# Kernel tuning notes

Measured on AMD Instinct MI355X. Metric: run time of the kernel, lower is better.

Reference implementation:

```python
import jax, jax.numpy as jnp
import numpy as np
from jax import lax

D_MODEL, N_STATE, L_LEN = 1024, 64, 4096
DT_INIT = 0.1


def hippo_legs_matrix(N):
    # Standard HiPPO-LegS: A[n,k] = -sqrt(2n+1)sqrt(2k+1) if n>k, -(n+1) if n==k, 0 else
    n = np.arange(N, dtype=np.float32)
    r = np.sqrt(2.0 * n + 1.0)
    A = np.where(n[:, None] > n[None, :], r[:, None] * r[None, :], 0.0)
    A = -(A + np.diag(n + 1.0))
    B = r.copy()
    return jnp.asarray(A, jnp.float32), jnp.asarray(B, jnp.float32)


def setup_inputs() -> dict:
    key = jax.random.key(0)
    kB, kC = jax.random.split(key)
    A_ct, B_ref = hippo_legs_matrix(N_STATE)
    B0 = jnp.tile(B_ref[None, :], (D_MODEL, 1))
    B = B0 + 0.01 * jax.random.normal(kB, (D_MODEL, N_STATE), jnp.float32)
    C = jax.random.normal(kC, (D_MODEL, N_STATE), jnp.float32) * 0.1
    D = jnp.zeros((D_MODEL,), jnp.float32)
    log_dt = jnp.asarray(np.log(DT_INIT), jnp.float32)
    return {"A_ct": A_ct, "B": B, "C": C, "D": D, "log_dt": log_dt}


def reference(A_ct, B, C, D, log_dt):
    dt = jnp.exp(log_dt)
    N = A_ct.shape[0]
    I = jnp.eye(N, dtype=A_ct.dtype)
    M = I - (dt / 2.0) * A_ct          # (N,N)
    P = I + (dt / 2.0) * A_ct          # (N,N)
    A_bar = jnp.linalg.solve(M, P)     # (N,N)
    # B_bar[d] = M^{-1} (dt * B[d])  -> solve on transposed batch
    B_bar = jnp.linalg.solve(M, (dt * B).T).T  # (D,N)

    def step(x, _):
        # x: (D,N) state; emit readout then advance
        y = jnp.sum(C * x, axis=-1)    # (D,)
        return x @ A_bar.T, y

    _, ys = lax.scan(step, B_bar, None, length=L_LEN)  # ys: (L,D)
    K = ys.T                                           # (D,L)
    K = K.at[:, 0].add(D)
    return K[:, None, :]                                # (D,1,L)
```

## Files before the change

### kernel.cpp

```cpp
#include <hip/hip_runtime.h>
#include <math.h>


#define BPAD 72

#define WS_BBAR   16
#define WS_SPL    65552
#define WS_MV     (WS_SPL + 12*8192)
#define WS_GT     (WS_MV + 4096)
#define WS_H      (WS_GT + 64*4096)
#define WS_W      (WS_H + 64*4096)
#define WS_X      (WS_W + 1024*4096)

using bf16x8 = __attribute__((ext_vector_type(8))) short;
using f32x4v = __attribute__((ext_vector_type(4))) float;
typedef unsigned short ushort_t;

__device__ __forceinline__ ushort_t f2bf(float x) {
  unsigned u = __builtin_bit_cast(unsigned, x);
  return (ushort_t)((u + 0x7FFFu + ((u >> 16) & 1u)) >> 16);
}
__device__ __forceinline__ float bfhi(float x) {
  unsigned u = __builtin_bit_cast(unsigned, x);
  unsigned r = (u + 0x7FFFu + ((u >> 16) & 1u)) & 0xFFFF0000u;
  return __builtin_bit_cast(float, r);
}
__device__ __forceinline__ ushort_t* usp(float* ws, int foff) {
  return (ushort_t*)(ws + foff);
}
__device__ __forceinline__ const ushort_t* uspc(const float* ws, int foff) {
  return (const ushort_t*)(ws + foff);
}

__device__ __forceinline__ void mm_frag(const ushort_t* __restrict__ Ah,
                                        const ushort_t* __restrict__ Al,
                                        const ushort_t* __restrict__ Bh,
                                        const ushort_t* __restrict__ Bl,
                                        int w, int lane, f32x4v acc[4]) {
  const int lm = lane & 15, quad = lane >> 4;
  const int ar = (16 * w + lm) * BPAD, ko = quad * 8;
#pragma unroll
  for (int nt = 0; nt < 4; ++nt) { acc[nt][0] = acc[nt][1] = acc[nt][2] = acc[nt][3] = 0.f; }
#pragma unroll
  for (int kc = 0; kc < 64; kc += 32) {
    const bf16x8 ahi = *(const bf16x8*)&Ah[ar + kc + ko];
    const bf16x8 alo = *(const bf16x8*)&Al[ar + kc + ko];
#pragma unroll
    for (int nt = 0; nt < 4; ++nt) {
      const int br = (16 * nt + lm) * BPAD + kc + ko;
      const bf16x8 bhi = *(const bf16x8*)&Bh[br];
      const bf16x8 blo = *(const bf16x8*)&Bl[br];
      acc[nt] = __builtin_amdgcn_mfma_f32_16x16x32_bf16(ahi, bhi, acc[nt], 0, 0, 0);
      acc[nt] = __builtin_amdgcn_mfma_f32_16x16x32_bf16(ahi, blo, acc[nt], 0, 0, 0);
      acc[nt] = __builtin_amdgcn_mfma_f32_16x16x32_bf16(alo, bhi, acc[nt], 0, 0, 0);
    }
  }
}

__device__ __forceinline__ void dstore_lds(const f32x4v acc[4],
                                           ushort_t* __restrict__ Ah, ushort_t* __restrict__ Al,
                                           ushort_t* __restrict__ Bth, ushort_t* __restrict__ Btl,
                                           int w, int lane) {
  const int lm = lane & 15, quad = lane >> 4;
#pragma unroll
  for (int nt = 0; nt < 4; ++nt) {
    const int n = 16 * nt + lm;
#pragma unroll
    for (int reg = 0; reg < 4; ++reg) {
      const int m = 16 * w + 4 * quad + reg;
      const float x = acc[nt][reg];
      const ushort_t h = f2bf(x), l = f2bf(x - bfhi(x));
      Ah[m * BPAD + n] = h; Al[m * BPAD + n] = l;
      Bth[n * BPAD + m] = h; Btl[n * BPAD + m] = l;
    }
  }
}

__device__ __forceinline__ void cp_l2w(const ushort_t* __restrict__ l,
                                       ushort_t* __restrict__ g, int tid) {
  for (int e = tid; e < 512; e += 256) {
    const int row = e >> 3, c8 = (e & 7) * 8;
    *(uint4*)&g[row * 64 + c8] = *(const uint4*)&l[row * BPAD + c8];
  }
}
__device__ __forceinline__ void cp_w2l(const ushort_t* __restrict__ g,
                                       ushort_t* __restrict__ l, int tid) {
  for (int e = tid; e < 512; e += 256) {
    const int row = e >> 3, c8 = (e & 7) * 8;
    *(uint4*)&l[row * BPAD + c8] = *(const uint4*)&g[row * 64 + c8];
  }
}

__device__ __forceinline__ void split_stage(const float* __restrict__ g,
                                            ushort_t* __restrict__ Ah,
                                            ushort_t* __restrict__ Al, int tid) {
#pragma unroll
  for (int j = 0; j < 4; ++j) {
    const int flat = j * 1024 + tid * 4;
    const int row = flat >> 6, col = flat & 63;
    const float4 v = *(const float4*)&g[flat];
    ushort_t h0 = f2bf(v.x), h1 = f2bf(v.y), h2 = f2bf(v.z), h3 = f2bf(v.w);
    ushort_t l0 = f2bf(v.x - bfhi(v.x)), l1 = f2bf(v.y - bfhi(v.y));
    ushort_t l2 = f2bf(v.z - bfhi(v.z)), l3 = f2bf(v.w - bfhi(v.w));
    uint2 hp, lp;
    hp.x = (unsigned)h0 | ((unsigned)h1 << 16); hp.y = (unsigned)h2 | ((unsigned)h3 << 16);
    lp.x = (unsigned)l0 | ((unsigned)l1 << 16); lp.y = (unsigned)l2 | ((unsigned)l3 << 16);
    *(uint2*)&Ah[row * BPAD + col] = hp;
    *(uint2*)&Al[row * BPAD + col] = lp;
  }
}

#define ARR (64 * BPAD)

__global__ __launch_bounds__(256) void k_setup(const float* __restrict__ A,
                                               const float* __restrict__ logdt,
                                               float* __restrict__ ws) {
  __shared__ __align__(16) char SM[74240];
  float* Msh = (float*)SM;
  float* Tm  = (float*)(SM + 16640);
  float* tmpb = (float*)(SM + 33280);
  ushort_t* ping = (ushort_t*)(SM + 37376);
  ushort_t* pong = (ushort_t*)SM;
  const int tid = threadIdx.x;
  const int w = tid >> 6, lane = tid & 63;

  const float hdt = 0.5f * expf(logdt[0]);
  for (int idx = tid; idx < 4096; idx += 256) {
    const int i = idx >> 6, j = idx & 63;
    Msh[i * 65 + j] = ((i == j) ? 1.f : 0.f) - hdt * A[idx];
    Tm[i * 65 + j] = 0.f;
  }
  __syncthreads();
  if (tid < 64) Tm[tid * 65 + tid] = 1.0f / Msh[tid * 65 + tid];
  __syncthreads();
  for (int lb = 0; lb < 6; ++lb) {
    const int b = 1 << lb;
    const int E = 32 * b;
    for (int e = tid; e < E; e += 256) {
      const int rem = e & (b * b - 1);
      const int p = e >> (2 * lb);
      const int i = rem >> lb, j = rem & (b - 1);
      const int c0 = p << (lb + 1), r0 = c0 + b;
      float s = 0.f;
      for (int k = 0; k < b; ++k)
        s += Msh[(r0 + i) * 65 + c0 + k] * Tm[(c0 + k) * 65 + c0 + j];
      tmpb[e] = s;
    }
    __syncthreads();
    for (int e = tid; e < E; e += 256) {
      const int rem = e & (b * b - 1);
      const int p = e >> (2 * lb);
      const int i = rem >> lb, j = rem & (b - 1);
      const int c0 = p << (lb + 1), r0 = c0 + b;
      float s = 0.f;
      const float* tp = &tmpb[e - rem];
      for (int k = 0; k < b; ++k)
        s += Tm[(r0 + i) * 65 + r0 + k] * tp[k * b + j];
      Tm[(r0 + i) * 65 + c0 + j] = -s;
    }
    __syncthreads();
  }

  {
    ushort_t* MvH = usp(ws, WS_MV);
    ushort_t* MvL = usp(ws, WS_MV + 2048);
    for (int idx = tid; idx < 4096; idx += 256) {
      const int i = idx >> 6, j = idx & 63;
      const float mv = Tm[i * 65 + j];
      MvH[idx] = f2bf(mv); MvL[idx] = f2bf(mv - bfhi(mv));
      const float v = 2.f * mv - ((i == j) ? 1.f : 0.f);
      const ushort_t h = f2bf(v), l = f2bf(v - bfhi(v));
      ping[0 * ARR + i * BPAD + j] = h; ping[1 * ARR + i * BPAD + j] = l;
      ping[2 * ARR + j * BPAD + i] = h; ping[3 * ARR + j * BPAD + i] = l;
    }
  }
  __syncthreads();
  cp_l2w(ping + 0 * ARR, usp(ws, WS_SPL + 0), tid);
  cp_l2w(ping + 1 * ARR, usp(ws, WS_SPL + 2048), tid);
  cp_l2w(ping + 2 * ARR, usp(ws, WS_SPL + 4096), tid);
  cp_l2w(ping + 3 * ARR, usp(ws, WS_SPL + 6144), tid);

  ushort_t* cur = ping;
  ushort_t* nxt = pong;
  for (int sj = 1; sj < 12; ++sj) {
    f32x4v acc[4];
    mm_frag(cur, cur + ARR, cur + 2 * ARR, cur + 3 * ARR, w, lane, acc);
    dstore_lds(acc, nxt, nxt + ARR, nxt + 2 * ARR, nxt + 3 * ARR, w, lane);
    __syncthreads();
    const int base = WS_SPL + sj * 8192;
    cp_l2w(nxt + 0 * ARR, usp(ws, base + 0), tid);
    cp_l2w(nxt + 1 * ARR, usp(ws, base + 2048), tid);
    cp_l2w(nxt + 2 * ARR, usp(ws, base + 4096), tid);
    cp_l2w(nxt + 3 * ARR, usp(ws, base + 6144), tid);
    ushort_t* t = cur; cur = nxt; nxt = t;
  }
}

__global__ __launch_bounds__(256) void k_powers(const float* __restrict__ Bg,
                                                const float* __restrict__ logdt,
                                                float* __restrict__ ws) {
  __shared__ __align__(16) ushort_t SMp[8 * ARR];
  ushort_t* curA = SMp;
  ushort_t* ponA = SMp + 2 * ARR;
  ushort_t* Bst  = SMp + 4 * ARR;
  ushort_t* BtO  = SMp + 6 * ARR;
  const int p = blockIdx.x, tid = threadIdx.x;
  const int w = tid >> 6, lane = tid & 63;

  if (p < 128) {
    const int chain = p >> 6, r = p & 63;
    ushort_t* dstH = usp(ws, (chain ? WS_H : WS_GT) + r * 4096);
    ushort_t* dstL = usp(ws, (chain ? WS_H : WS_GT) + r * 4096 + 2048);
    if (r == 0) {
      for (int idx = tid; idx < 4096; idx += 256) {
        const int i = idx >> 6, j = idx & 63;
        dstH[idx] = (i == j) ? (ushort_t)0x3F80 : (ushort_t)0;
        dstL[idx] = 0;
      }
      return;
    }
    const int j0 = __ffs(r) - 1;
    if (r == (1 << j0)) {
      const int sb = WS_SPL + (chain * 6 + j0) * 8192;
      const int src = chain ? sb : (sb + 4096);
      const uint4* sh = (const uint4*)uspc(ws, src);
      const uint4* sl = (const uint4*)uspc(ws, src + 2048);
      uint4* dh = (uint4*)dstH;
      uint4* dl = (uint4*)dstL;
      for (int e = tid; e < 512; e += 256) { dh[e] = sh[e]; dl[e] = sl[e]; }
      return;
    }
    {
      const int sb = WS_SPL + (chain * 6 + j0) * 8192;
      cp_w2l(uspc(ws, sb + 0), curA, tid);
      cp_w2l(uspc(ws, sb + 2048), curA + ARR, tid);
    }
    ushort_t* ca = curA;
    ushort_t* na = ponA;
    for (int j = j0 + 1; j < 6; ++j) {
      if ((r >> j) & 1) {
        __syncthreads();
        const int sb = WS_SPL + (chain * 6 + j) * 8192;
        cp_w2l(uspc(ws, sb + 4096), Bst, tid);
        cp_w2l(uspc(ws, sb + 6144), Bst + ARR, tid);
        __syncthreads();
        f32x4v acc[4];
        mm_frag(ca, ca + ARR, Bst, Bst + ARR, w, lane, acc);
        dstore_lds(acc, na, na + ARR, BtO, BtO + ARR, w, lane);
        ushort_t* t = ca; ca = na; na = t;
      }
    }
    __syncthreads();
    if (chain == 0) {
      cp_l2w(BtO, dstH, tid);
      cp_l2w(BtO + ARR, dstL, tid);
    } else {
      cp_l2w(ca, dstH, tid);
      cp_l2w(ca + ARR, dstL, tid);
    }
  } else {
    const int d0 = (p - 128) * 64;
    const float dtv = expf(logdt[0]);
    split_stage(Bg + d0 * 64, curA, curA + ARR, tid);
    cp_w2l(uspc(ws, WS_MV), Bst, tid);
    cp_w2l(uspc(ws, WS_MV + 2048), Bst + ARR, tid);
    __syncthreads();
    f32x4v acc[4];
    mm_frag(curA, curA + ARR, Bst, Bst + ARR, w, lane, acc);
    const int lm = lane & 15, quad = lane >> 4;
    float* od = ws + WS_BBAR + d0 * 64;
#pragma unroll
    for (int nt = 0; nt < 4; ++nt)
#pragma unroll
      for (int reg = 0; reg < 4; ++reg)
        od[(16 * w + 4 * quad + reg) * 64 + 16 * nt + lm] = dtv * acc[nt][reg];
  }
}

__global__ __launch_bounds__(256) void k_expand(const float* __restrict__ Cg,
                                                float* __restrict__ ws) {
  __shared__ __align__(16) ushort_t SMe[4 * ARR];
  ushort_t* Asp = SMe;
  ushort_t* Bsp = SMe + 2 * ARR;
  const int p = blockIdx.x, tid = threadIdx.x;
  const int chain = p >> 10, rr = (p >> 4) & 63, dch = p & 15;
  const int w = tid >> 6, lane = tid & 63;
  const int d0 = dch * 64;

  split_stage(chain ? (ws + WS_BBAR + d0 * 64) : (Cg + d0 * 64), Asp, Asp + ARR, tid);
  const int mb = (chain ? WS_H : WS_GT) + rr * 4096;
  cp_w2l(uspc(ws, mb + 0), Bsp, tid);
  cp_w2l(uspc(ws, mb + 2048), Bsp + ARR, tid);
  __syncthreads();

  f32x4v acc[4];
  mm_frag(Asp, Asp + ARR, Bsp, Bsp + ARR, w, lane, acc);

  const int lm = lane & 15, quad = lane >> 4;
  float* dst = ws + (chain ? WS_X : WS_W) + d0 * 4096 + rr * 64;
#pragma unroll
  for (int nt = 0; nt < 4; ++nt)
#pragma unroll
    for (int reg = 0; reg < 4; ++reg)
      dst[(16 * w + 4 * quad + reg) * 4096 + 16 * nt + lm] = acc[nt][reg];
}

__global__ __launch_bounds__(256) void k_contract(const float* __restrict__ Dg,
                                                  const float* __restrict__ ws,
                                                  float* __restrict__ out) {
  __shared__ __align__(16) ushort_t XhiL[64 * BPAD];
  __shared__ __align__(16) ushort_t XloL[64 * BPAD];
  __shared__ __align__(16) ushort_t WhiL[64 * BPAD];
  __shared__ __align__(16) ushort_t WloL[64 * BPAD];
  const int d = blockIdx.x, tid = threadIdx.x;
  const float* Wg = ws + WS_W + d * 4096;
  const float* Xg = ws + WS_X + d * 4096;

#pragma unroll
  for (int j = 0; j < 4; ++j) {
    const int flat = j * 1024 + tid * 4;
    const int row = flat >> 6, col = flat & 63;
    const float4 wv = *(const float4*)&Wg[flat];
    const float4 xv = *(const float4*)&Xg[flat];
    const int o = row * BPAD + col;
#pragma unroll
    for (int s = 0; s < 2; ++s) {
      const float4 v = s ? xv : wv;
      ushort_t h0 = f2bf(v.x), h1 = f2bf(v.y), h2 = f2bf(v.z), h3 = f2bf(v.w);
      ushort_t l0 = f2bf(v.x - bfhi(v.x)), l1 = f2bf(v.y - bfhi(v.y));
      ushort_t l2 = f2bf(v.z - bfhi(v.z)), l3 = f2bf(v.w - bfhi(v.w));
      uint2 hp, lp;
      hp.x = (unsigned)h0 | ((unsigned)h1 << 16); hp.y = (unsigned)h2 | ((unsigned)h3 << 16);
      lp.x = (unsigned)l0 | ((unsigned)l1 << 16); lp.y = (unsigned)l2 | ((unsigned)l3 << 16);
      *(uint2*)&(s ? XhiL : WhiL)[o] = hp;
      *(uint2*)&(s ? XloL : WloL)[o] = lp;
    }
  }
  __syncthreads();

  const int w = tid >> 6, lane = tid & 63;
  const int lm = lane & 15, quad = lane >> 4;
  const int qrow = 16 * w + lm;
  const int koff = quad * 8;

  f32x4v acc[4];
#pragma unroll
  for (int nt = 0; nt < 4; ++nt) { acc[nt][0] = 0.f; acc[nt][1] = 0.f; acc[nt][2] = 0.f; acc[nt][3] = 0.f; }

#pragma unroll
  for (int kc = 0; kc < 64; kc += 32) {
    const bf16x8 ahi = *(const bf16x8*)&XhiL[qrow * BPAD + kc + koff];
    const bf16x8 alo = *(const bf16x8*)&XloL[qrow * BPAD + kc + koff];
#pragma unroll
    for (int nt = 0; nt < 4; ++nt) {
      const int rrow = 16 * nt + lm;
      const bf16x8 bhi = *(const bf16x8*)&WhiL[rrow * BPAD + kc + koff];
      const bf16x8 blo = *(const bf16x8*)&WloL[rrow * BPAD + kc + koff];
      acc[nt] = __builtin_amdgcn_mfma_f32_16x16x32_bf16(ahi, bhi, acc[nt], 0, 0, 0);
      acc[nt] = __builtin_amdgcn_mfma_f32_16x16x32_bf16(ahi, blo, acc[nt], 0, 0, 0);
      acc[nt] = __builtin_amdgcn_mfma_f32_16x16x32_bf16(alo, bhi, acc[nt], 0, 0, 0);
    }
  }

  if (tid == 0) acc[0][0] += Dg[d];

  float* od = out + d * 4096;
#pragma unroll
  for (int nt = 0; nt < 4; ++nt) {
#pragma unroll
    for (int reg = 0; reg < 4; ++reg) {
      const int q = 16 * w + quad * 4 + reg;
      od[q * 64 + 16 * nt + lm] = acc[nt][reg];
    }
  }
}

extern "C" void kernel_launch(void* const* d_in, const int* in_sizes, int n_in,
                              void* d_out, int out_size, void* d_ws, size_t ws_size,
                              hipStream_t stream) {
  const float* A     = (const float*)d_in[0];
  const float* B     = (const float*)d_in[1];
  const float* C     = (const float*)d_in[2];
  const float* Dv    = (const float*)d_in[3];
  const float* logdt = (const float*)d_in[4];
  float* ws  = (float*)d_ws;
  float* out = (float*)d_out;

  hipLaunchKernelGGL(k_setup,    dim3(1),    dim3(256), 0, stream, A, logdt, ws);
  hipLaunchKernelGGL(k_powers,   dim3(144),  dim3(256), 0, stream, B, logdt, ws);
  hipLaunchKernelGGL(k_expand,   dim3(2048), dim3(256), 0, stream, C, ws);
  hipLaunchKernelGGL(k_contract, dim3(1024), dim3(256), 0, stream, Dv, ws, out);
}
```

Measured before the change: 127.9 us.

## Load MFMA fragments directly from global memory and reuse B tiles in expand

Removes LDS staging across k_powers, k_expand and k_contract: MFMA operand fragments are now loaded straight from global or workspace memory and split into bf16 hi/lo in registers via a new helper. k_expand now keeps the power-matrix fragments in registers and loops over four d-chunks per block, so its grid shrinks from 2048 to 512 blocks. dstore_lds packs its transposed stores into uint2 writes. The change drops LDS round-trips and barriers, but in exchange it relies on uncoalesced global loads and gives expand less parallelism.

```diff
diff --git a/kernel.cpp b/kernel.cpp
--- a/kernel.cpp
+++ b/kernel.cpp
@@ -3,6 +3,7 @@
 
 
 #define BPAD 72
+#define ARR (64 * BPAD)
 
 #define WS_BBAR   16
 #define WS_SPL    65552
@@ -32,6 +33,18 @@
   return (const ushort_t*)(ws + foff);
 }
 
+__device__ __forceinline__ void ldsplit8(const float* __restrict__ p,
+                                         bf16x8& h, bf16x8& l) {
+  const float4 a = *(const float4*)p;
+  const float4 b = *(const float4*)(p + 4);
+  const float v[8] = {a.x, a.y, a.z, a.w, b.x, b.y, b.z, b.w};
+#pragma unroll
+  for (int i = 0; i < 8; ++i) {
+    h[i] = (short)f2bf(v[i]);
+    l[i] = (short)f2bf(v[i] - bfhi(v[i]));
+  }
+}
+
 __device__ __forceinline__ void mm_frag(const ushort_t* __restrict__ Ah,
                                         const ushort_t* __restrict__ Al,
                                         const ushort_t* __restrict__ Bh,
@@ -62,17 +75,25 @@
                                            ushort_t* __restrict__ Bth, ushort_t* __restrict__ Btl,
                                            int w, int lane) {
   const int lm = lane & 15, quad = lane >> 4;
+  const int m0 = 16 * w + 4 * quad;
 #pragma unroll
   for (int nt = 0; nt < 4; ++nt) {
     const int n = 16 * nt + lm;
+    ushort_t h[4], l[4];
 #pragma unroll
     for (int reg = 0; reg < 4; ++reg) {
-      const int m = 16 * w + 4 * quad + reg;
       const float x = acc[nt][reg];
-      const ushort_t h = f2bf(x), l = f2bf(x - bfhi(x));
-      Ah[m * BPAD + n] = h; Al[m * BPAD + n] = l;
-      Bth[n * BPAD + m] = h; Btl[n * BPAD + m] = l;
-    }
+      h[reg] = f2bf(x); l[reg] = f2bf(x - bfhi(x));
+      Ah[(m0 + reg) * BPAD + n] = h[reg];
+      Al[(m0 + reg) * BPAD + n] = l[reg];
+    }
+    uint2 hp, lp;
+    hp.x = (unsigned)h[0] | ((unsigned)h[1] << 16);
+    hp.y = (unsigned)h[2] | ((unsigned)h[3] << 16);
+    lp.x = (unsigned)l[0] | ((unsigned)l[1] << 16);
+    lp.y = (unsigned)l[2] | ((unsigned)l[3] << 16);
+    *(uint2*)&Bth[n * BPAD + m0] = hp;
+    *(uint2*)&Btl[n * BPAD + m0] = lp;
   }
 }
 
@@ -83,34 +104,6 @@
     *(uint4*)&g[row * 64 + c8] = *(const uint4*)&l[row * BPAD + c8];
   }
 }
-__device__ __forceinline__ void cp_w2l(const ushort_t* __restrict__ g,
-                                       ushort_t* __restrict__ l, int tid) {
-  for (int e = tid; e < 512; e += 256) {
-    const int row = e >> 3, c8 = (e & 7) * 8;
-    *(uint4*)&l[row * BPAD + c8] = *(const uint4*)&g[row * 64 + c8];
-  }
-}
-
-__device__ __forceinline__ void split_stage(const float* __restrict__ g,
-                                            ushort_t* __restrict__ Ah,
-                                            ushort_t* __restrict__ Al, int tid) {
-#pragma unroll
-  for (int j = 0; j < 4; ++j) {
-    const int flat = j * 1024 + tid * 4;
-    const int row = flat >> 6, col = flat & 63;
-    const float4 v = *(const float4*)&g[flat];
-    ushort_t h0 = f2bf(v.x), h1 = f2bf(v.y), h2 = f2bf(v.z), h3 = f2bf(v.w);
-    ushort_t l0 = f2bf(v.x - bfhi(v.x)), l1 = f2bf(v.y - bfhi(v.y));
-    ushort_t l2 = f2bf(v.z - bfhi(v.z)), l3 = f2bf(v.w - bfhi(v.w));
-    uint2 hp, lp;
-    hp.x = (unsigned)h0 | ((unsigned)h1 << 16); hp.y = (unsigned)h2 | ((unsigned)h3 << 16);
-    lp.x = (unsigned)l0 | ((unsigned)l1 << 16); lp.y = (unsigned)l2 | ((unsigned)l3 << 16);
-    *(uint2*)&Ah[row * BPAD + col] = hp;
-    *(uint2*)&Al[row * BPAD + col] = lp;
-  }
-}
-
-#define ARR (64 * BPAD)
 
 __global__ __launch_bounds__(256) void k_setup(const float* __restrict__ A,
                                                const float* __restrict__ logdt,
@@ -199,13 +192,10 @@
 __global__ __launch_bounds__(256) void k_powers(const float* __restrict__ Bg,
                                                 const float* __restrict__ logdt,
                                                 float* __restrict__ ws) {
-  __shared__ __align__(16) ushort_t SMp[8 * ARR];
-  ushort_t* curA = SMp;
-  ushort_t* ponA = SMp + 2 * ARR;
-  ushort_t* Bst  = SMp + 4 * ARR;
-  ushort_t* BtO  = SMp + 6 * ARR;
+  __shared__ __align__(16) ushort_t Pl[4 * ARR];
   const int p = blockIdx.x, tid = threadIdx.x;
   const int w = tid >> 6, lane = tid & 63;
+  const int lm = lane & 15, quad = lane >> 4;
 
   if (p < 128) {
     const int chain = p >> 6, r = p & 63;
@@ -230,44 +220,114 @@
       for (int e = tid; e < 512; e += 256) { dh[e] = sh[e]; dl[e] = sl[e]; }
       return;
     }
-    {
-      const int sb = WS_SPL + (chain * 6 + j0) * 8192;
-      cp_w2l(uspc(ws, sb + 0), curA, tid);
-      cp_w2l(uspc(ws, sb + 2048), curA + ARR, tid);
-    }
-    ushort_t* ca = curA;
-    ushort_t* na = ponA;
+    const int sb0 = WS_SPL + (chain * 6 + j0) * 8192;
+    const ushort_t* A0h = uspc(ws, sb0);
+    const ushort_t* A0l = uspc(ws, sb0 + 2048);
+    int cur = -1;
     for (int j = j0 + 1; j < 6; ++j) {
-      if ((r >> j) & 1) {
+      if (!((r >> j) & 1)) continue;
+      const int sb = WS_SPL + (chain * 6 + j) * 8192;
+      const ushort_t* BtH = uspc(ws, sb + 4096);
+      const ushort_t* BtL = uspc(ws, sb + 6144);
+      f32x4v acc[4];
+#pragma unroll
+      for (int nt = 0; nt < 4; ++nt) { acc[nt][0] = acc[nt][1] = acc[nt][2] = acc[nt][3] = 0.f; }
+#pragma unroll
+      for (int c = 0; c < 2; ++c) {
+        bf16x8 ahi, alo;
+        if (cur < 0) {
+          const int off = (16 * w + lm) * 64 + c * 32 + quad * 8;
+          ahi = *(const bf16x8*)&A0h[off];
+          alo = *(const bf16x8*)&A0l[off];
+        } else {
+          const ushort_t* Ph = Pl + cur * 2 * ARR;
+          const int off = (16 * w + lm) * BPAD + c * 32 + quad * 8;
+          ahi = *(const bf16x8*)&Ph[off];
+          alo = *(const bf16x8*)&Ph[ARR + off];
+        }
+#pragma unroll
+        for (int nt = 0; nt < 4; ++nt) {
+          const int off = (16 * nt + lm) * 64 + c * 32 + quad * 8;
+          const bf16x8 bh = *(const bf16x8*)&BtH[off];
+          const bf16x8 bl = *(const bf16x8*)&BtL[off];
+          acc[nt] = __builtin_amdgcn_mfma_f32_16x16x32_bf16(ahi, bh, acc[nt], 0, 0, 0);
+          acc[nt] = __builtin_amdgcn_mfma_f32_16x16x32_bf16(ahi, bl, acc[nt], 0, 0, 0);
+          acc[nt] = __builtin_amdgcn_mfma_f32_16x16x32_bf16(alo, bh, acc[nt], 0, 0, 0);
+        }
+      }
+      if (r >> (j + 1)) {
+        const int nb = (cur < 0) ? 0 : (cur ^ 1);
+        ushort_t* Ph = Pl + nb * 2 * ARR;
+#pragma unroll
+        for (int nt = 0; nt < 4; ++nt) {
+          const int n = 16 * nt + lm;
+#pragma unroll
+          for (int reg = 0; reg < 4; ++reg) {
+            const int m = 16 * w + 4 * quad + reg;
+            const float x = acc[nt][reg];
+            Ph[m * BPAD + n] = f2bf(x);
+            Ph[ARR + m * BPAD + n] = f2bf(x - bfhi(x));
+          }
+        }
         __syncthreads();
-        const int sb = WS_SPL + (chain * 6 + j) * 8192;
-        cp_w2l(uspc(ws, sb + 4096), Bst, tid);
-        cp_w2l(uspc(ws, sb + 6144), Bst + ARR, tid);
-        __syncthreads();
-        f32x4v acc[4];
-        mm_frag(ca, ca + ARR, Bst, Bst + ARR, w, lane, acc);
-        dstore_lds(acc, na, na + ARR, BtO, BtO + ARR, w, lane);
-        ushort_t* t = ca; ca = na; na = t;
+        cur = nb;
+      } else {
+        if (chain == 0) {
+          const int m0 = 16 * w + 4 * quad;
+#pragma unroll
+          for (int nt = 0; nt < 4; ++nt) {
+            const int n = 16 * nt + lm;
+            ushort_t h[4], l[4];
+#pragma unroll
+            for (int reg = 0; reg < 4; ++reg) {
+              const float x = acc[nt][reg];
+              h[reg] = f2bf(x); l[reg] = f2bf(x - bfhi(x));
+            }
+            uint2 hp, lp;
+            hp.x = (unsigned)h[0] | ((unsigned)h[1] << 16);
+            hp.y = (unsigned)h[2] | ((unsigned)h[3] << 16);
+            lp.x = (unsigned)l[0] | ((unsigned)l[1] << 16);
+            lp.y = (unsigned)l[2] | ((unsigned)l[3] << 16);
+            *(uint2*)&dstH[n * 64 + m0] = hp;
+            *(uint2*)&dstL[n * 64 + m0] = lp;
+          }
+        } else {
+#pragma unroll
+          for (int nt = 0; nt < 4; ++nt) {
+            const int n = 16 * nt + lm;
+#pragma unroll
+            for (int reg = 0; reg < 4; ++reg) {
+              const int m = 16 * w + 4 * quad + reg;
+              const float x = acc[nt][reg];
+              dstH[m * 64 + n] = f2bf(x);
+              dstL[m * 64 + n] = f2bf(x - bfhi(x));
+            }
+          }
+        }
       }
-    }
-    __syncthreads();
-    if (chain == 0) {
-      cp_l2w(BtO, dstH, tid);
-      cp_l2w(BtO + ARR, dstL, tid);
-    } else {
-      cp_l2w(ca, dstH, tid);
-      cp_l2w(ca + ARR, dstL, tid);
     }
   } else {
     const int d0 = (p - 128) * 64;
     const float dtv = expf(logdt[0]);
-    split_stage(Bg + d0 * 64, curA, curA + ARR, tid);
-    cp_w2l(uspc(ws, WS_MV), Bst, tid);
-    cp_w2l(uspc(ws, WS_MV + 2048), Bst + ARR, tid);
-    __syncthreads();
+    const ushort_t* MvH = uspc(ws, WS_MV);
+    const ushort_t* MvL = uspc(ws, WS_MV + 2048);
     f32x4v acc[4];
-    mm_frag(curA, curA + ARR, Bst, Bst + ARR, w, lane, acc);
-    const int lm = lane & 15, quad = lane >> 4;
+#pragma unroll
+    for (int nt = 0; nt < 4; ++nt) { acc[nt][0] = acc[nt][1] = acc[nt][2] = acc[nt][3] = 0.f; }
+#pragma unroll
+    for (int c = 0; c < 2; ++c) {
+      bf16x8 ahi, alo;
+      ldsplit8(&Bg[(d0 + 16 * w + lm) * 64 + c * 32 + quad * 8], ahi, alo);
+#pragma unroll
+      for (int nt = 0; nt < 4; ++nt) {
+        const int off = (16 * nt + lm) * 64 + c * 32 + quad * 8;
+        const bf16x8 bh = *(const bf16x8*)&MvH[off];
+        const bf16x8 bl = *(const bf16x8*)&MvL[off];
+        acc[nt] = __builtin_amdgcn_mfma_f32_16x16x32_bf16(ahi, bh, acc[nt], 0, 0, 0);
+        acc[nt] = __builtin_amdgcn_mfma_f32_16x16x32_bf16(ahi, bl, acc[nt], 0, 0, 0);
+        acc[nt] = __builtin_amdgcn_mfma_f32_16x16x32_bf16(alo, bh, acc[nt], 0, 0, 0);
+      }
+    }
     float* od = ws + WS_BBAR + d0 * 64;
 #pragma unroll
     for (int nt = 0; nt < 4; ++nt)
@@ -279,83 +339,70 @@
 
 __global__ __launch_bounds__(256) void k_expand(const float* __restrict__ Cg,
                                                 float* __restrict__ ws) {
-  __shared__ __align__(16) ushort_t SMe[4 * ARR];
-  ushort_t* Asp = SMe;
-  ushort_t* Bsp = SMe + 2 * ARR;
   const int p = blockIdx.x, tid = threadIdx.x;
-  const int chain = p >> 10, rr = (p >> 4) & 63, dch = p & 15;
+  const int chain = p >> 8, rr = (p >> 2) & 63, dgrp = p & 3;
   const int w = tid >> 6, lane = tid & 63;
-  const int d0 = dch * 64;
-
-  split_stage(chain ? (ws + WS_BBAR + d0 * 64) : (Cg + d0 * 64), Asp, Asp + ARR, tid);
+  const int lm = lane & 15, quad = lane >> 4;
   const int mb = (chain ? WS_H : WS_GT) + rr * 4096;
-  cp_w2l(uspc(ws, mb + 0), Bsp, tid);
-  cp_w2l(uspc(ws, mb + 2048), Bsp + ARR, tid);
-  __syncthreads();
-
-  f32x4v acc[4];
-  mm_frag(Asp, Asp + ARR, Bsp, Bsp + ARR, w, lane, acc);
-
-  const int lm = lane & 15, quad = lane >> 4;
-  float* dst = ws + (chain ? WS_X : WS_W) + d0 * 4096 + rr * 64;
-#pragma unroll
-  for (int nt = 0; nt < 4; ++nt)
-#pragma unroll
-    for (int reg = 0; reg < 4; ++reg)
-      dst[(16 * w + 4 * quad + reg) * 4096 + 16 * nt + lm] = acc[nt][reg];
+  const ushort_t* BtH = uspc(ws, mb);
+  const ushort_t* BtL = uspc(ws, mb + 2048);
+
+  bf16x8 bhi[2][4], blo[2][4];
+#pragma unroll
+  for (int c = 0; c < 2; ++c)
+#pragma unroll
+    for (int nt = 0; nt < 4; ++nt) {
+      const int off = (16 * nt + lm) * 64 + c * 32 + quad * 8;
+      bhi[c][nt] = *(const bf16x8*)&BtH[off];
+      blo[c][nt] = *(const bf16x8*)&BtL[off];
+    }
+
+  for (int g = 0; g < 4; ++g) {
+    const int d0 = (dgrp * 4 + g) * 64;
+    const float* src = chain ? (ws + WS_BBAR + d0 * 64) : (Cg + d0 * 64);
+    f32x4v acc[4];
+#pragma unroll
+    for (int nt = 0; nt < 4; ++nt) { acc[nt][0] = acc[nt][1] = acc[nt][2] = acc[nt][3] = 0.f; }
+#pragma unroll
+    for (int c = 0; c < 2; ++c) {
+      bf16x8 ahi, alo;
+      ldsplit8(&src[(16 * w + lm) * 64 + c * 32 + quad * 8], ahi, alo);
+#pragma unroll
+      for (int nt = 0; nt < 4; ++nt) {
+        acc[nt] = __builtin_amdgcn_mfma_f32_16x16x32_bf16(ahi, bhi[c][nt], acc[nt], 0, 0, 0);
+        acc[nt] = __builtin_amdgcn_mfma_f32_16x16x32_bf16(ahi, blo[c][nt], acc[nt], 0, 0, 0);
+        acc[nt] = __builtin_amdgcn_mfma_f32_16x16x32_bf16(alo, bhi[c][nt], acc[nt], 0, 0, 0);
+      }
+    }
+    float* dst = ws + (chain ? WS_X : WS_W) + d0 * 4096 + rr * 64;
+#pragma unroll
+    for (int nt = 0; nt < 4; ++nt)
+#pragma unroll
+      for (int reg = 0; reg < 4; ++reg)
+        dst[(16 * w + 4 * quad + reg) * 4096 + 16 * nt + lm] = acc[nt][reg];
+  }
 }
 
 __global__ __launch_bounds__(256) void k_contract(const float* __restrict__ Dg,
                                                   const float* __restrict__ ws,
                                                   float* __restrict__ out) {
-  __shared__ __align__(16) ushort_t XhiL[64 * BPAD];
-  __shared__ __align__(16) ushort_t XloL[64 * BPAD];
-  __shared__ __align__(16) ushort_t WhiL[64 * BPAD];
-  __shared__ __align__(16) ushort_t WloL[64 * BPAD];
   const int d = blockIdx.x, tid = threadIdx.x;
-  const float* Wg = ws + WS_W + d * 4096;
-  const float* Xg = ws + WS_X + d * 4096;
-
-#pragma unroll
-  for (int j = 0; j < 4; ++j) {
-    const int flat = j * 1024 + tid * 4;
-    const int row = flat >> 6, col = flat & 63;
-    const float4 wv = *(const float4*)&Wg[flat];
-    const float4 xv = *(const float4*)&Xg[flat];
-    const int o = row * BPAD + col;
-#pragma unroll
-    for (int s = 0; s < 2; ++s) {
-      const float4 v = s ? xv : wv;
-      ushort_t h0 = f2bf(v.x), h1 = f2bf(v.y), h2 = f2bf(v.z), h3 = f2bf(v.w);
-      ushort_t l0 = f2bf(v.x - bfhi(v.x)), l1 = f2bf(v.y - bfhi(v.y));
-      ushort_t l2 = f2bf(v.z - bfhi(v.z)), l3 = f2bf(v.w - bfhi(v.w));
-      uint2 hp, lp;
-      hp.x = (unsigned)h0 | ((unsigned)h1 << 16); hp.y = (unsigned)h2 | ((unsigned)h3 << 16);
-      lp.x = (unsigned)l0 | ((unsigned)l1 << 16); lp.y = (unsigned)l2 | ((unsigned)l3 << 16);
-      *(uint2*)&(s ? XhiL : WhiL)[o] = hp;
-      *(uint2*)&(s ? XloL : WloL)[o] = lp;
-    }
-  }
-  __syncthreads();
-
   const int w = tid >> 6, lane = tid & 63;
   const int lm = lane & 15, quad = lane >> 4;
-  const int qrow = 16 * w + lm;
-  const int koff = quad * 8;
+  const float* Xg = ws + WS_X + d * 4096;
+  const float* Wg = ws + WS_W + d * 4096;
 
   f32x4v acc[4];
 #pragma unroll
-  for (int nt = 0; nt < 4; ++nt) { acc[nt][0] = 0.f; acc[nt][1] = 0.f; acc[nt][2] = 0.f; acc[nt][3] = 0.f; }
-
-#pragma unroll
-  for (int kc = 0; kc < 64; kc += 32) {
-    const bf16x8 ahi = *(const bf16x8*)&XhiL[qrow * BPAD + kc + koff];
-    const bf16x8 alo = *(const bf16x8*)&XloL[qrow * BPAD + kc + koff];
+  for (int nt = 0; nt < 4; ++nt) { acc[nt][0] = acc[nt][1] = acc[nt][2] = acc[nt][3] = 0.f; }
+#pragma unroll
+  for (int c = 0; c < 2; ++c) {
+    bf16x8 ahi, alo;
+    ldsplit8(&Xg[(16 * w + lm) * 64 + c * 32 + quad * 8], ahi, alo);
 #pragma unroll
     for (int nt = 0; nt < 4; ++nt) {
-      const int rrow = 16 * nt + lm;
-      const bf16x8 bhi = *(const bf16x8*)&WhiL[rrow * BPAD + kc + koff];
-      const bf16x8 blo = *(const bf16x8*)&WloL[rrow * BPAD + kc + koff];
+      bf16x8 bhi, blo;
+      ldsplit8(&Wg[(16 * nt + lm) * 64 + c * 32 + quad * 8], bhi, blo);
       acc[nt] = __builtin_amdgcn_mfma_f32_16x16x32_bf16(ahi, bhi, acc[nt], 0, 0, 0);
       acc[nt] = __builtin_amdgcn_mfma_f32_16x16x32_bf16(ahi, blo, acc[nt], 0, 0, 0);
       acc[nt] = __builtin_amdgcn_mfma_f32_16x16x32_bf16(alo, bhi, acc[nt], 0, 0, 0);
@@ -388,6 +435,6 @@
 
   hipLaunchKernelGGL(k_setup,    dim3(1),    dim3(256), 0, stream, A, logdt, ws);
   hipLaunchKernelGGL(k_powers,   dim3(144),  dim3(256), 0, stream, B, logdt, ws);
-  hipLaunchKernelGGL(k_expand,   dim3(2048), dim3(256), 0, stream, C, ws);
+  hipLaunchKernelGGL(k_expand,   dim3(512),  dim3(256), 0, stream, C, ws);
   hipLaunchKernelGGL(k_contract, dim3(1024), dim3(256), 0, stream, Dv, ws, out);
 }
```

Result: slower. 135.5 us (+5.9%).
